# Performance work log

Hardware: AMD Instinct MI355X
Metric: run time of the kernel (lower is better)

## Reference

```python
import jax, jax.numpy as jnp
import numpy as np

NUM_HEADS = 16
ROPE_THETA = 10000.0


def _rope(x, pos):
    # x: [B, H, S, d_k], pos: [S]
    d_k = x.shape[-1]
    inv_freq = ROPE_THETA ** (-jnp.arange(0, d_k, 2, dtype=x.dtype) / d_k)  # [d_k/2]
    ang = pos[:, None].astype(x.dtype) * inv_freq[None, :]  # [S, d_k/2]
    cos, sin = jnp.cos(ang), jnp.sin(ang)
    x1 = x[..., 0::2]
    x2 = x[..., 1::2]
    r1 = x1 * cos - x2 * sin
    r2 = x1 * sin + x2 * cos
    return jnp.stack([r1, r2], axis=-1).reshape(x.shape)


def setup_inputs() -> dict:
    key = jax.random.key(0)
    kx, kq, kk, kv = jax.random.split(key, 4)
    B, S, D = 2, 2048, 2048
    scale = 1.0 / np.sqrt(D)
    x = jax.random.normal(kx, (B, S, D), dtype=jnp.float32)
    wq = jax.random.normal(kq, (D, D), dtype=jnp.float32) * scale
    wk = jax.random.normal(kk, (D, D), dtype=jnp.float32) * scale
    wv = jax.random.normal(kv, (D, D), dtype=jnp.float32) * scale
    return {"x": x, "wq": wq, "wk": wk, "wv": wv}


def reference(x, wq, wk, wv):
    B, S, D = x.shape
    H = NUM_HEADS
    d_k = D // H
    # QKV projections (Linear stores weight as [out, in]; y = x @ W^T)
    q = (x @ wq.T).reshape(B, S, H, d_k).transpose(0, 2, 1, 3)  # [B,H,S,dk]
    k = (x @ wk.T).reshape(B, S, H, d_k).transpose(0, 2, 1, 3)
    v = (x @ wv.T).reshape(B, S, H, d_k).transpose(0, 2, 1, 3)
    pos = jnp.arange(S)
    q = _rope(q, pos)
    k = _rope(k, pos)
    scores = jnp.einsum("bhqd,bhkd->bhqk", q, k) / jnp.sqrt(jnp.asarray(d_k, x.dtype))
    causal = jnp.tril(jnp.ones((S, S), dtype=bool))
    scores = jnp.where(causal, scores, jnp.asarray(-1e9, x.dtype))
    attn = jax.nn.softmax(scores, axis=-1)
    out = jnp.einsum("bhqk,bhkd->bhqd", attn, v)  # [B,H,S,dk]
    return out.transpose(0, 2, 1, 3).reshape(B, S, D)
```

## Files before the change

kernel.cpp:

```cpp
#include <hip/hip_runtime.h>
#include <stdint.h>

typedef unsigned short u16;
typedef __bf16 bf16x8 __attribute__((ext_vector_type(8)));
typedef float f32x4 __attribute__((ext_vector_type(4)));
typedef float f32x16 __attribute__((ext_vector_type(16)));

#define NHEADS 16
#define DKH    128
#define SEQ    2048
#define DMODEL 2048
#define NBATCH 2

typedef const __attribute__((address_space(1))) void* gas1_t;
typedef __attribute__((address_space(3))) void* las3_t;

__device__ __forceinline__ void gload_lds16(const void* g, void* l) {
  __builtin_amdgcn_global_load_lds((gas1_t)(uintptr_t)g,
                                   (las3_t)(uint32_t)(uintptr_t)l, 16, 0, 0);
}

__device__ __forceinline__ u16 bf(float f) {
  return __builtin_bit_cast(u16, (__bf16)f);
}

__device__ __forceinline__ uint32_t pk(float lo, float hi) {
  return (uint32_t)bf(lo) | ((uint32_t)bf(hi) << 16);
}

__device__ __forceinline__ float lanebcast(int srclane, float v) {
  return __builtin_bit_cast(float,
      __builtin_amdgcn_ds_bpermute(srclane << 2, __builtin_bit_cast(int, v)));
}

__global__ __launch_bounds__(256) void cvt_all(const float* __restrict__ x,
                                               const float* __restrict__ wq,
                                               const float* __restrict__ wk,
                                               const float* __restrict__ wv,
                                               u16* __restrict__ xb,
                                               u16* __restrict__ wb) {
  int i = (blockIdx.x * 256 + threadIdx.x) * 4;
  const int NX = NBATCH * SEQ * DMODEL;
  const int NW = DMODEL * DMODEL;
  const float* src;
  u16* dst;
  int j;
  if (i < NX) { src = x; dst = xb; j = i; }
  else {
    int k = i - NX;
    int w = k / NW;
    j = k - w * NW;
    src = (w == 0) ? wq : (w == 1) ? wk : wv;
    dst = wb + (size_t)w * NW;
  }
  const float4 v = *(const float4*)(src + j);
  uint2 o;
  o.x = (uint32_t)bf(v.x) | ((uint32_t)bf(v.y) << 16);
  o.y = (uint32_t)bf(v.z) | ((uint32_t)bf(v.w) << 16);
  *(uint2*)(dst + j) = o;
}

__global__ __launch_bounds__(256) void rope_table(float2* __restrict__ tbl) {
  int i = blockIdx.x * 256 + threadIdx.x;
  int s = i >> 6, d2 = i & 63;
  const float kLog2Theta = 13.28771237954945f;
  float inv_freq = exp2f(-(float)d2 * (2.0f / 128.0f) * kLog2Theta);
  float ang = (float)s * inv_freq;
  tbl[i] = make_float2(cosf(ang), sinf(ang));
}

__global__ __launch_bounds__(256, 4) void gemm_qkv(const u16* __restrict__ Abf,
                                                   const u16* __restrict__ Wbf,
                                                   const float2* __restrict__ rope,
                                                   u16* __restrict__ qb,
                                                   u16* __restrict__ kb,
                                                   u16* __restrict__ vtb) {
  __shared__ u16 S[16384];
  u16* As = S;
  u16* Bs = S + 8192;
  const int tid = threadIdx.x;
  const int lane = tid & 63, wid = tid >> 6;
  const int wr = wid >> 1, wc = wid & 1;
  const int blk = blockIdx.x;
  const int m0 = (blk / 48) * 128;
  const int n0 = (blk % 48) * 128;
  const int lrow = lane & 15, lgrp = lane >> 4, lko = lgrp * 8;
  const int rswz = (lrow & 7) << 3;

  const int srow = tid >> 3;
  const int scol = ((tid & 7) * 8) ^ (((tid >> 3) & 7) << 3);

  f32x4 acc[4][4] = {};

  for (int k0 = 0; k0 < DMODEL; k0 += 64) {
    __syncthreads();
#pragma unroll
    for (int c = 0; c < 4; ++c) {
      gload_lds16(Abf + (size_t)(m0 + c * 32 + srow) * DMODEL + k0 + scol,
                  As + (c * 256 + tid) * 8);
      gload_lds16(Wbf + (size_t)(n0 + c * 32 + srow) * DMODEL + k0 + scol,
                  Bs + (c * 256 + tid) * 8);
    }
    __syncthreads();
#pragma unroll
    for (int kk = 0; kk < 2; ++kk) {
      const int rc = (kk * 32 + lko) ^ rswz;
      bf16x8 a[4], b[4];
#pragma unroll
      for (int m = 0; m < 4; ++m)
        a[m] = *(const bf16x8*)(As + (wr * 64 + m * 16 + lrow) * 64 + rc);
#pragma unroll
      for (int n = 0; n < 4; ++n)
        b[n] = *(const bf16x8*)(Bs + (wc * 64 + n * 16 + lrow) * 64 + rc);
#pragma unroll
      for (int m = 0; m < 4; ++m)
#pragma unroll
        for (int n = 0; n < 4; ++n)
          acc[m][n] = __builtin_amdgcn_mfma_f32_16x16x32_bf16(a[m], b[n], acc[m][n], 0, 0, 0);
    }
  }

  const int sel = n0 >> 11;
  const float qsc = 0.08838834764831845f * 1.44269504088896341f;

  if (sel != 2) {
#pragma unroll
    for (int m = 0; m < 4; ++m) {
      int grow0 = m0 + wr * 64 + m * 16 + (lgrp << 2);
#pragma unroll
      for (int n = 0; n < 4; ++n) {
        int gcol = n0 + wc * 64 + n * 16 + lrow;
        int within = gcol & 2047;
        int h_ = within >> 7, d_ = within & 127;
#pragma unroll
        for (int j = 0; j < 4; ++j) {
          float v = acc[m][n][j];
          int r = grow0 + j;
          int b_ = r >> 11, s_ = r & 2047;
          int bh = b_ * NHEADS + h_;
          float part = __shfl_xor(v, 1);
          float2 cs2 = rope[s_ * 64 + (d_ >> 1)];
          v = (d_ & 1) ? (part * cs2.y + v * cs2.x) : (v * cs2.x - part * cs2.y);
          if (sel == 0) v *= qsc;
          u16* dq = sel ? kb : qb;
          dq[((size_t)bh * SEQ + s_) * DKH + d_] = bf(v);
        }
      }
    }
  } else {
    __syncthreads();
#pragma unroll
    for (int m = 0; m < 4; ++m) {
      int sl0 = wr * 64 + m * 16 + (lgrp << 2);
#pragma unroll
      for (int n = 0; n < 4; ++n) {
        int dcol = wc * 64 + n * 16 + lrow;
        const int dx = (dcol & 7) << 4;
#pragma unroll
        for (int j = 0; j < 4; ++j)
          S[dcol * 128 + ((sl0 + j) ^ dx)] = bf(acc[m][n][j]);
      }
    }
    __syncthreads();
    const int b_ = m0 >> 11, s0 = m0 & 2047;
    const int h_ = (n0 >> 7) & 15;
    const int bh = b_ * NHEADS + h_;
    const int d = tid >> 1, hf = tid & 1;
    const int dx = (d & 7) << 4;
    u16* grow = vtb + ((size_t)bh * DKH + d) * SEQ + s0 + hf * 64;
#pragma unroll
    for (int g = 0; g < 8; ++g) {
      bf16x8 v8 = *(const bf16x8*)(S + d * 128 + ((hf * 64 + g * 8) ^ dx));
      *(bf16x8*)(grow + g * 8) = v8;
    }
  }
}

__global__ __launch_bounds__(256, 2) void attn_fwd(const u16* __restrict__ qb,
                                                   const u16* __restrict__ kb,
                                                   const u16* __restrict__ vtb,
                                                   float* __restrict__ out) {
  __shared__ u16 Ks[2][64 * 128];
  __shared__ u16 Vs[2][128 * 64];
  const int tid = threadIdx.x, lane = tid & 63, wid = tid >> 6;
  const int blk = blockIdx.x;
  const int r_ = blk & 255, half = blk >> 8;
  const int bh = r_ & 31;
  const int pairidx = r_ >> 5;
  const int chunk = half ? (15 - pairidx) : pairidx;
  const int qln = lane & 31, hi = lane >> 5;
  const int hi4 = hi << 2, hi8 = hi << 3;
  const int kswz = (qln & 15) << 3;
  const int vswz = (qln & 7) << 3;

  const int krow_l = tid >> 4;
  const int kcol = (((tid & 15) ^ (tid >> 4)) << 3);
  const int vrow_l = tid >> 3;
  const int vcol = (((tid & 7) ^ ((tid >> 3) & 7)) << 3);

  const int b_ = bh >> 4, h_ = bh & 15;
  const size_t kbase = (size_t)bh * SEQ;
  const size_t vbase = (size_t)bh * DKH;

#define STAGE_KV(bufi, kv_)                                                  \
  _Pragma("unroll")                                                          \
  for (int c = 0; c < 4; ++c) {                                              \
    gload_lds16(kb + (kbase + (kv_) + c * 16 + krow_l) * DKH + kcol,         \
                &Ks[bufi][(c * 256 + tid) * 8]);                             \
    gload_lds16(vtb + (vbase + c * 32 + vrow_l) * SEQ + (kv_) + vcol,        \
                &Vs[bufi][(c * 256 + tid) * 8]);                             \
  }

  const int q0w = chunk * 128 + wid * 32;
  const int qglob = q0w + qln;

  bf16x8 qa[8];
#pragma unroll
  for (int kd = 0; kd < 8; ++kd)
    qa[kd] = *(const bf16x8*)(qb + (kbase + q0w + qln) * DKH + kd * 16 + hi8);

  f32x16 o[4] = {};
  float mrun = -1e30f, lrun = 0.f;

  const int nt = 2 * chunk + 2;

  STAGE_KV(0, 0);
  __syncthreads();

#pragma unroll 1
  for (int t = 0; t < nt; ++t) {
    const int cur = t & 1;
    if (t + 1 < nt) { STAGE_KV(cur ^ 1, (t + 1) * 64); }
    const int kv0 = t * 64;

    if (kv0 <= q0w + 31) {
      const u16* Kb = &Ks[cur][0];
      const u16* Vb = &Vs[cur][0];

      f32x16 sfv[2] = {};
      __builtin_amdgcn_s_setprio(1);
#pragma unroll
      for (int kd = 0; kd < 8; ++kd)
#pragma unroll
        for (int st = 0; st < 2; ++st) {
          bf16x8 kf = *(const bf16x8*)(Kb + (st * 32 + qln) * 128 +
                                       ((kd * 16 + hi8) ^ kswz));
          sfv[st] = __builtin_amdgcn_mfma_f32_32x32x16_bf16(kf, qa[kd], sfv[st], 0, 0, 0);
        }
      __builtin_amdgcn_s_setprio(0);

      if (kv0 + 63 > q0w) {
#pragma unroll
        for (int st = 0; st < 2; ++st)
#pragma unroll
          for (int r = 0; r < 16; ++r)
            if (kv0 + st * 32 + ((r & 3) + 8 * (r >> 2)) + hi4 > qglob)
              sfv[st][r] = -1e30f;
      }

      float tm[16];
#pragma unroll
      for (int r = 0; r < 16; ++r) tm[r] = fmaxf(sfv[0][r], sfv[1][r]);
#pragma unroll
      for (int r = 0; r < 8; ++r) tm[r] = fmaxf(tm[r], tm[r + 8]);
#pragma unroll
      for (int r = 0; r < 4; ++r) tm[r] = fmaxf(tm[r], tm[r + 4]);
      float m_ = fmaxf(fmaxf(tm[0], tm[1]), fmaxf(tm[2], tm[3]));
      m_ = fmaxf(m_, __shfl_xor(m_, 32));

      if (__any(m_ > mrun + 11.5f)) {
        float mnew = fmaxf(mrun, m_);
        float alpha = __builtin_amdgcn_exp2f(mrun - mnew);
        mrun = mnew;
        lrun *= alpha;
#pragma unroll
        for (int r = 0; r < 16; ++r) {
          float ar = lanebcast((r & 3) + 8 * (r >> 2) + hi4, alpha);
          o[0][r] *= ar; o[1][r] *= ar; o[2][r] *= ar; o[3][r] *= ar;
        }
      }

#pragma unroll
      for (int st = 0; st < 2; ++st)
#pragma unroll
        for (int r = 0; r < 16; ++r)
          sfv[st][r] = __builtin_amdgcn_exp2f(sfv[st][r] - mrun);
      float ts[16];
#pragma unroll
      for (int r = 0; r < 16; ++r) ts[r] = sfv[0][r] + sfv[1][r];
#pragma unroll
      for (int r = 0; r < 8; ++r) ts[r] += ts[r + 8];
#pragma unroll
      for (int r = 0; r < 4; ++r) ts[r] += ts[r + 4];
      float sum = (ts[0] + ts[1]) + (ts[2] + ts[3]);
      sum += __shfl_xor(sum, 32);
      lrun += sum;

      __builtin_amdgcn_s_setprio(1);
#pragma unroll
      for (int ks = 0; ks < 4; ++ks) {
        const int st = ks >> 1, rb = (ks & 1) * 8;
        uint32_t w0 = pk(sfv[st][rb + 0], sfv[st][rb + 1]);
        uint32_t w1 = pk(sfv[st][rb + 2], sfv[st][rb + 3]);
        uint32_t w2 = pk(sfv[st][rb + 4], sfv[st][rb + 5]);
        uint32_t w3 = pk(sfv[st][rb + 6], sfv[st][rb + 7]);
        uint32_t s0 = hi ? w0 : w2, s1 = hi ? w1 : w3;
        uint32_t r0 = (uint32_t)__shfl_xor((int)s0, 32);
        uint32_t r1 = (uint32_t)__shfl_xor((int)s1, 32);
        union { uint32_t u[4]; bf16x8 v; } pa;
        pa.u[0] = hi ? r0 : w0;
        pa.u[1] = hi ? r1 : w1;
        pa.u[2] = hi ? w2 : r0;
        pa.u[3] = hi ? w3 : r1;
#pragma unroll
        for (int d0 = 0; d0 < 4; ++d0) {
          bf16x8 vf = *(const bf16x8*)(Vb + (d0 * 32 + qln) * 64 +
                                       ((ks * 16 + hi8) ^ vswz));
          o[d0] = __builtin_amdgcn_mfma_f32_32x32x16_bf16(pa.v, vf, o[d0], 0, 0, 0);
        }
      }
      __builtin_amdgcn_s_setprio(0);
    }

    __syncthreads();
  }

  float inv = 1.f / lrun;
#pragma unroll
  for (int r = 0; r < 16; ++r) {
    const int qr = (r & 3) + 8 * (r >> 2) + hi4;
    float invr = lanebcast(qr, inv);
    float* op = out + ((size_t)b_ * SEQ + q0w + qr) * DMODEL + h_ * DKH + qln;
    op[0]  = o[0][r] * invr;
    op[32] = o[1][r] * invr;
    op[64] = o[2][r] * invr;
    op[96] = o[3][r] * invr;
  }
#undef STAGE_KV
}

extern "C" void kernel_launch(void* const* d_in, const int* in_sizes, int n_in,
                              void* d_out, int out_size, void* d_ws, size_t ws_size,
                              hipStream_t stream) {
  const float* x  = (const float*)d_in[0];
  const float* wq = (const float*)d_in[1];
  const float* wk = (const float*)d_in[2];
  const float* wv = (const float*)d_in[3];
  float* out = (float*)d_out;
  char* ws = (char*)d_ws;

  u16* xb  = (u16*)(ws);
  u16* wb  = (u16*)(ws + 16777216);
  u16* qb  = (u16*)(ws + 41943040);
  u16* kb  = (u16*)(ws + 58720256);
  u16* vtb = (u16*)(ws + 75497472);

  float2* rope = (float2*)d_out;

  rope_table<<<512, 256, 0, stream>>>(rope);
  cvt_all<<<20480, 256, 0, stream>>>(x, wq, wk, wv, xb, wb);
  gemm_qkv<<<1536, 256, 0, stream>>>(xb, wb, rope, qb, kb, vtb);
  attn_fwd<<<512, 256, 0, stream>>>(qb, kb, vtb, out);
}
```

Baseline: 191.7 us.

## Enlarge QKV GEMM tiles to 256x256 with double-buffered LDS prefetch

Rewrites the QKV projection GEMM to use 256x256 output tiles per 512-thread block, with a double-buffered LDS pipeline that prefetches the next K slice while MFMAs run. It also raises MFMA priority via setprio and remaps block indices across groups of eight for better L2 locality. The epilogues are adjusted for the larger tile, including a V transpose that now spans two heads. The aim is more operand reuse per load and latency hidden by overlap, at the cost of 128KB of LDS, heavier register pressure and many barriers per iteration.

Measured after the change: 213.2 us. 11.2% more time.

```diff
diff --git a/kernel.cpp b/kernel.cpp
--- a/kernel.cpp
+++ b/kernel.cpp
@@ -69,64 +69,107 @@
   tbl[i] = make_float2(cosf(ang), sinf(ang));
 }
 
-__global__ __launch_bounds__(256, 4) void gemm_qkv(const u16* __restrict__ Abf,
+__global__ __launch_bounds__(512, 2) void gemm_qkv(const u16* __restrict__ Abf,
                                                    const u16* __restrict__ Wbf,
                                                    const float2* __restrict__ rope,
                                                    u16* __restrict__ qb,
                                                    u16* __restrict__ kb,
                                                    u16* __restrict__ vtb) {
-  __shared__ u16 S[16384];
-  u16* As = S;
-  u16* Bs = S + 8192;
+  __shared__ u16 SH[65536];
+
   const int tid = threadIdx.x;
   const int lane = tid & 63, wid = tid >> 6;
-  const int wr = wid >> 1, wc = wid & 1;
-  const int blk = blockIdx.x;
-  const int m0 = (blk / 48) * 128;
-  const int n0 = (blk % 48) * 128;
-  const int lrow = lane & 15, lgrp = lane >> 4, lko = lgrp * 8;
+  const int wr = wid >> 2, wc = wid & 3;
+  const int g = (blockIdx.x & 7) * 48 + (blockIdx.x >> 3);
+  const int m0 = (g / 24) * 256;
+  const int n0 = (g % 24) * 256;
+  const int lrow = lane & 15, lgrp = lane >> 4;
   const int rswz = (lrow & 7) << 3;
 
-  const int srow = tid >> 3;
-  const int scol = ((tid & 7) * 8) ^ (((tid >> 3) & 7) << 3);
-
-  f32x4 acc[4][4] = {};
-
-  for (int k0 = 0; k0 < DMODEL; k0 += 64) {
-    __syncthreads();
-#pragma unroll
-    for (int c = 0; c < 4; ++c) {
-      gload_lds16(Abf + (size_t)(m0 + c * 32 + srow) * DMODEL + k0 + scol,
-                  As + (c * 256 + tid) * 8);
-      gload_lds16(Wbf + (size_t)(n0 + c * 32 + srow) * DMODEL + k0 + scol,
-                  Bs + (c * 256 + tid) * 8);
-    }
-    __syncthreads();
-#pragma unroll
-    for (int kk = 0; kk < 2; ++kk) {
-      const int rc = (kk * 32 + lko) ^ rswz;
-      bf16x8 a[4], b[4];
-#pragma unroll
-      for (int m = 0; m < 4; ++m)
-        a[m] = *(const bf16x8*)(As + (wr * 64 + m * 16 + lrow) * 64 + rc);
-#pragma unroll
-      for (int n = 0; n < 4; ++n)
-        b[n] = *(const bf16x8*)(Bs + (wc * 64 + n * 16 + lrow) * 64 + rc);
-#pragma unroll
-      for (int m = 0; m < 4; ++m)
-#pragma unroll
-        for (int n = 0; n < 4; ++n)
-          acc[m][n] = __builtin_amdgcn_mfma_f32_16x16x32_bf16(a[m], b[n], acc[m][n], 0, 0, 0);
-    }
-  }
-
-  const int sel = n0 >> 11;
+  const int srow8 = tid >> 3;
+  const int scol = ((tid & 7) ^ (srow8 & 7)) << 3;
+
+  const u16* const Ag = Abf + (size_t)m0 * DMODEL;
+  const u16* const Bg = Wbf + (size_t)n0 * DMODEL;
+
+  f32x4 acc[8][4] = {};
+
+#define STAGE_A(buf, k0_, c)                                                  \
+  gload_lds16(Ag + (size_t)((c) * 64 + srow8) * DMODEL + (k0_) + scol,        \
+              SH + (buf) * 16384 + (c) * 4096 + tid * 8)
+#define STAGE_B(buf, k0_, c)                                                  \
+  gload_lds16(Bg + (size_t)((c) * 64 + srow8) * DMODEL + (k0_) + scol,        \
+              SH + 32768 + (buf) * 16384 + (c) * 4096 + tid * 8)
+#define LDA(base, row, kk)                                                    \
+  (*(const bf16x8*)((base) + (row) * 64 + (((kk) * 32 + lgrp * 8) ^ rswz)))
+#define MFMA16(mh)                                                            \
+  __builtin_amdgcn_s_setprio(1);                                              \
+  _Pragma("unroll") for (int m_ = 0; m_ < 4; ++m_)                            \
+    _Pragma("unroll") for (int n_ = 0; n_ < 4; ++n_)                          \
+      acc[(mh) * 4 + m_][n_] = __builtin_amdgcn_mfma_f32_16x16x32_bf16(       \
+          a[m_], b[n_], acc[(mh) * 4 + m_][n_], 0, 0, 0);                     \
+  __builtin_amdgcn_s_setprio(0)
+
+#pragma unroll
+  for (int c = 0; c < 4; ++c) { STAGE_A(0, 0, c); STAGE_B(0, 0, c); }
+  asm volatile("s_waitcnt vmcnt(0)" ::: "memory");
+  __builtin_amdgcn_s_barrier();
+
+  const int NT = DMODEL / 64;
+#pragma unroll 1
+  for (int t = 0; t < NT; ++t) {
+    const int cur = t & 1, nxt = cur ^ 1;
+    const int k1 = (t + 1) * 64;
+    const u16* Ab = SH + cur * 16384;
+    const u16* Bb = SH + 32768 + cur * 16384;
+    const bool pf = (t + 1 < NT);
+    bf16x8 a[4], b[4];
+
+#pragma unroll
+    for (int m = 0; m < 4; ++m) a[m] = LDA(Ab, wr * 128 + m * 16 + lrow, 0);
+#pragma unroll
+    for (int n = 0; n < 4; ++n) b[n] = LDA(Bb, wc * 64 + n * 16 + lrow, 0);
+    if (pf) { STAGE_A(nxt, k1, 0); STAGE_A(nxt, k1, 1);
+              STAGE_B(nxt, k1, 0); STAGE_B(nxt, k1, 1); }
+    __builtin_amdgcn_s_barrier();
+    MFMA16(0);
+    __builtin_amdgcn_s_barrier();
+
+#pragma unroll
+    for (int m = 0; m < 4; ++m) a[m] = LDA(Ab, wr * 128 + 64 + m * 16 + lrow, 0);
+    if (pf) { STAGE_A(nxt, k1, 2); STAGE_A(nxt, k1, 3);
+              STAGE_B(nxt, k1, 2); STAGE_B(nxt, k1, 3); }
+    __builtin_amdgcn_s_barrier();
+    MFMA16(1);
+    __builtin_amdgcn_s_barrier();
+
+#pragma unroll
+    for (int m = 0; m < 4; ++m) a[m] = LDA(Ab, wr * 128 + m * 16 + lrow, 1);
+#pragma unroll
+    for (int n = 0; n < 4; ++n) b[n] = LDA(Bb, wc * 64 + n * 16 + lrow, 1);
+    __builtin_amdgcn_s_barrier();
+    MFMA16(0);
+    __builtin_amdgcn_s_barrier();
+
+#pragma unroll
+    for (int m = 0; m < 4; ++m) a[m] = LDA(Ab, wr * 128 + 64 + m * 16 + lrow, 1);
+    __builtin_amdgcn_s_barrier();
+    MFMA16(1);
+    asm volatile("s_waitcnt vmcnt(0)" ::: "memory");
+    __builtin_amdgcn_s_barrier();
+  }
+#undef STAGE_A
+#undef STAGE_B
+#undef LDA
+#undef MFMA16
+
+  const int sel = (n0 >= 4096) ? 2 : (n0 >= 2048 ? 1 : 0);
   const float qsc = 0.08838834764831845f * 1.44269504088896341f;
 
   if (sel != 2) {
 #pragma unroll
-    for (int m = 0; m < 4; ++m) {
-      int grow0 = m0 + wr * 64 + m * 16 + (lgrp << 2);
+    for (int m = 0; m < 8; ++m) {
+      int grow0 = m0 + wr * 128 + m * 16 + (lgrp << 2);
 #pragma unroll
       for (int n = 0; n < 4; ++n) {
         int gcol = n0 + wc * 64 + n * 16 + lrow;
@@ -150,28 +193,28 @@
   } else {
     __syncthreads();
 #pragma unroll
-    for (int m = 0; m < 4; ++m) {
-      int sl0 = wr * 64 + m * 16 + (lgrp << 2);
+    for (int m = 0; m < 8; ++m) {
+      int sl0 = wr * 128 + m * 16 + (lgrp << 2);
 #pragma unroll
       for (int n = 0; n < 4; ++n) {
         int dcol = wc * 64 + n * 16 + lrow;
-        const int dx = (dcol & 7) << 4;
+        const int dx = (dcol & 7) << 3;
 #pragma unroll
         for (int j = 0; j < 4; ++j)
-          S[dcol * 128 + ((sl0 + j) ^ dx)] = bf(acc[m][n][j]);
+          SH[dcol * 256 + ((sl0 + j) ^ dx)] = bf(acc[m][n][j]);
       }
     }
     __syncthreads();
     const int b_ = m0 >> 11, s0 = m0 & 2047;
-    const int h_ = (n0 >> 7) & 15;
-    const int bh = b_ * NHEADS + h_;
+    const int h0 = (n0 & 2047) >> 7;
     const int d = tid >> 1, hf = tid & 1;
-    const int dx = (d & 7) << 4;
-    u16* grow = vtb + ((size_t)bh * DKH + d) * SEQ + s0 + hf * 64;
-#pragma unroll
-    for (int g = 0; g < 8; ++g) {
-      bf16x8 v8 = *(const bf16x8*)(S + d * 128 + ((hf * 64 + g * 8) ^ dx));
-      *(bf16x8*)(grow + g * 8) = v8;
+    const int dx = (d & 7) << 3;
+    const int bh = b_ * NHEADS + h0 + (d >> 7);
+    u16* grow = vtb + ((size_t)bh * DKH + (d & 127)) * SEQ + s0 + hf * 128;
+#pragma unroll
+    for (int gi = 0; gi < 16; ++gi) {
+      bf16x8 v8 = *(const bf16x8*)(SH + d * 256 + ((hf * 128 + gi * 8) ^ dx));
+      *(bf16x8*)(grow + gi * 8) = v8;
     }
   }
 }
@@ -359,6 +402,6 @@
 
   rope_table<<<512, 256, 0, stream>>>(rope);
   cvt_all<<<20480, 256, 0, stream>>>(x, wq, wk, wv, xb, wb);
-  gemm_qkv<<<1536, 256, 0, stream>>>(xb, wb, rope, qb, kb, vtb);
+  gemm_qkv<<<384, 512, 0, stream>>>(xb, wb, rope, qb, kb, vtb);
   attn_fwd<<<512, 256, 0, stream>>>(qb, kb, vtb, out);
 }
```

## Triple-buffer QKV GEMM with 256x128 tiles, 512 threads and XCD-aware block mapping

Applied to the files above, without the earlier changes.

Rewrites the QKV projection GEMM to use 256x128 block tiles with 8 waves and a three-stage LDS ring buffer. Global-to-LDS prefetches for tile t+2 are interleaved with the MFMA phases, using vmcnt waits and raw barriers, with raised wave priority around the MFMAs. Blocks are remapped so each XCD handles a contiguous range of N tiles, which should improve L2 reuse of the weights. The V-transpose epilogue is adapted to the larger M tile. This costs more LDS (144KB per block) and lower occupancy, and the hand-managed waitcnt logic risks races if the counts are wrong.

Measured after the change: 199.3 us. 4.0% more time.

```diff
diff --git a/kernel.cpp b/kernel.cpp
--- a/kernel.cpp
+++ b/kernel.cpp
@@ -69,58 +69,102 @@
   tbl[i] = make_float2(cosf(ang), sinf(ang));
 }
 
-__global__ __launch_bounds__(256, 4) void gemm_qkv(const u16* __restrict__ Abf,
+__global__ __launch_bounds__(512, 2) void gemm_qkv(const u16* __restrict__ Abf,
                                                    const u16* __restrict__ Wbf,
                                                    const float2* __restrict__ rope,
                                                    u16* __restrict__ qb,
                                                    u16* __restrict__ kb,
                                                    u16* __restrict__ vtb) {
-  __shared__ u16 S[16384];
-  u16* As = S;
-  u16* Bs = S + 8192;
+  __shared__ u16 SH[73728];
+
   const int tid = threadIdx.x;
   const int lane = tid & 63, wid = tid >> 6;
   const int wr = wid >> 1, wc = wid & 1;
-  const int blk = blockIdx.x;
-  const int m0 = (blk / 48) * 128;
-  const int n0 = (blk % 48) * 128;
-  const int lrow = lane & 15, lgrp = lane >> 4, lko = lgrp * 8;
+  const int xcd = blockIdx.x & 7, i_ = blockIdx.x >> 3;
+  const int m0 = (i_ / 6) * 256;
+  const int n0 = (xcd * 6 + (i_ % 6)) * 128;
+  const int lrow = lane & 15, lgrp = lane >> 4;
   const int rswz = (lrow & 7) << 3;
 
-  const int srow = tid >> 3;
-  const int scol = ((tid & 7) * 8) ^ (((tid >> 3) & 7) << 3);
+  const int srow8 = tid >> 3;
+  const int scol = ((tid & 7) ^ (srow8 & 7)) << 3;
+
+  const u16* const Ag = Abf + (size_t)m0 * DMODEL;
+  const u16* const Bg = Wbf + (size_t)n0 * DMODEL;
 
   f32x4 acc[4][4] = {};
 
-  for (int k0 = 0; k0 < DMODEL; k0 += 64) {
-    __syncthreads();
-#pragma unroll
-    for (int c = 0; c < 4; ++c) {
-      gload_lds16(Abf + (size_t)(m0 + c * 32 + srow) * DMODEL + k0 + scol,
-                  As + (c * 256 + tid) * 8);
-      gload_lds16(Wbf + (size_t)(n0 + c * 32 + srow) * DMODEL + k0 + scol,
-                  Bs + (c * 256 + tid) * 8);
-    }
-    __syncthreads();
-#pragma unroll
-    for (int kk = 0; kk < 2; ++kk) {
-      const int rc = (kk * 32 + lko) ^ rswz;
-      bf16x8 a[4], b[4];
-#pragma unroll
-      for (int m = 0; m < 4; ++m)
-        a[m] = *(const bf16x8*)(As + (wr * 64 + m * 16 + lrow) * 64 + rc);
+#define STAGE_A(buf, k0_, c)                                                  \
+  gload_lds16(Ag + (size_t)((c) * 64 + srow8) * DMODEL + (k0_) + scol,        \
+              SH + (buf) + (c) * 4096 + tid * 8)
+#define STAGE_B(buf, k0_, c)                                                  \
+  gload_lds16(Bg + (size_t)((c) * 64 + srow8) * DMODEL + (k0_) + scol,        \
+              SH + (buf) + 16384 + (c) * 4096 + tid * 8)
+#define LD8(base, row, kk)                                                    \
+  (*(const bf16x8*)((base) + (row) * 64 + (((kk) * 32 + lgrp * 8) ^ rswz)))
+
+#pragma unroll
+  for (int c = 0; c < 4; ++c) STAGE_A(0, 0, c);
+#pragma unroll
+  for (int c = 0; c < 2; ++c) STAGE_B(0, 0, c);
+#pragma unroll
+  for (int c = 0; c < 4; ++c) STAGE_A(24576, 64, c);
+#pragma unroll
+  for (int c = 0; c < 2; ++c) STAGE_B(24576, 64, c);
+  asm volatile("s_waitcnt vmcnt(6)" ::: "memory");
+  __builtin_amdgcn_s_barrier();
+
+  int bR = 0, bM = 24576, bW = 49152;
+  const int NT = DMODEL / 64;
+
+#pragma unroll 1
+  for (int t = 0; t < NT; ++t) {
+    const u16* Ar = SH + bR;
+    const u16* Br = SH + bR + 16384;
+    const int k2 = (t + 2) * 64;
+    const bool pf = (t + 2 < NT);
+    bf16x8 a[4], b[4];
+
+#pragma unroll
+    for (int m = 0; m < 4; ++m) a[m] = LD8(Ar, wr * 64 + m * 16 + lrow, 0);
+#pragma unroll
+    for (int n = 0; n < 4; ++n) b[n] = LD8(Br, wc * 64 + n * 16 + lrow, 0);
+    if (pf) { STAGE_A(bW, k2, 0); STAGE_A(bW, k2, 1); STAGE_A(bW, k2, 2); }
+    __builtin_amdgcn_s_barrier();
+    __builtin_amdgcn_s_setprio(1);
+#pragma unroll
+    for (int m = 0; m < 4; ++m)
 #pragma unroll
       for (int n = 0; n < 4; ++n)
-        b[n] = *(const bf16x8*)(Bs + (wc * 64 + n * 16 + lrow) * 64 + rc);
-#pragma unroll
-      for (int m = 0; m < 4; ++m)
-#pragma unroll
-        for (int n = 0; n < 4; ++n)
-          acc[m][n] = __builtin_amdgcn_mfma_f32_16x16x32_bf16(a[m], b[n], acc[m][n], 0, 0, 0);
-    }
-  }
-
-  const int sel = n0 >> 11;
+        acc[m][n] = __builtin_amdgcn_mfma_f32_16x16x32_bf16(a[m], b[n], acc[m][n], 0, 0, 0);
+    __builtin_amdgcn_s_setprio(0);
+    __builtin_amdgcn_s_barrier();
+
+#pragma unroll
+    for (int m = 0; m < 4; ++m) a[m] = LD8(Ar, wr * 64 + m * 16 + lrow, 1);
+#pragma unroll
+    for (int n = 0; n < 4; ++n) b[n] = LD8(Br, wc * 64 + n * 16 + lrow, 1);
+    if (pf) { STAGE_A(bW, k2, 3); STAGE_B(bW, k2, 0); STAGE_B(bW, k2, 1); }
+    __builtin_amdgcn_s_barrier();
+    __builtin_amdgcn_s_setprio(1);
+#pragma unroll
+    for (int m = 0; m < 4; ++m)
+#pragma unroll
+      for (int n = 0; n < 4; ++n)
+        acc[m][n] = __builtin_amdgcn_mfma_f32_16x16x32_bf16(a[m], b[n], acc[m][n], 0, 0, 0);
+    __builtin_amdgcn_s_setprio(0);
+    if (t < NT - 2) asm volatile("s_waitcnt vmcnt(6)" ::: "memory");
+    else            asm volatile("s_waitcnt vmcnt(0)" ::: "memory");
+    __builtin_amdgcn_s_barrier();
+
+    int tmp = bR; bR = bM; bM = bW; bW = tmp;
+  }
+#undef STAGE_A
+#undef STAGE_B
+#undef LD8
+
+  const int np = n0 >> 7;
+  const int sel = (np >= 32) ? 2 : (np >= 16 ? 1 : 0);
   const float qsc = 0.08838834764831845f * 1.44269504088896341f;
 
   if (sel != 2) {
@@ -155,22 +199,22 @@
 #pragma unroll
       for (int n = 0; n < 4; ++n) {
         int dcol = wc * 64 + n * 16 + lrow;
-        const int dx = (dcol & 7) << 4;
+        const int dx = (dcol & 7) << 3;
 #pragma unroll
         for (int j = 0; j < 4; ++j)
-          S[dcol * 128 + ((sl0 + j) ^ dx)] = bf(acc[m][n][j]);
+          SH[dcol * 256 + ((sl0 + j) ^ dx)] = bf(acc[m][n][j]);
       }
     }
     __syncthreads();
     const int b_ = m0 >> 11, s0 = m0 & 2047;
-    const int h_ = (n0 >> 7) & 15;
+    const int h_ = np & 15;
     const int bh = b_ * NHEADS + h_;
-    const int d = tid >> 1, hf = tid & 1;
-    const int dx = (d & 7) << 4;
-    u16* grow = vtb + ((size_t)bh * DKH + d) * SEQ + s0 + hf * 64;
+    const int d = tid >> 2, seg = tid & 3;
+    const int dxr = (d & 7) << 3;
+    u16* grow = vtb + ((size_t)bh * DKH + d) * SEQ + s0 + seg * 64;
 #pragma unroll
     for (int g = 0; g < 8; ++g) {
-      bf16x8 v8 = *(const bf16x8*)(S + d * 128 + ((hf * 64 + g * 8) ^ dx));
+      bf16x8 v8 = *(const bf16x8*)(SH + d * 256 + ((seg * 64 + g * 8) ^ dxr));
       *(bf16x8*)(grow + g * 8) = v8;
     }
   }
@@ -359,6 +403,6 @@
 
   rope_table<<<512, 256, 0, stream>>>(rope);
   cvt_all<<<20480, 256, 0, stream>>>(x, wq, wk, wv, xb, wb);
-  gemm_qkv<<<1536, 256, 0, stream>>>(xb, wb, rope, qb, kb, vtb);
+  gemm_qkv<<<768, 512, 0, stream>>>(xb, wb, rope, qb, kb, vtb);
   attn_fwd<<<512, 256, 0, stream>>>(qb, kb, vtb, out);
 }
```

## Read K/V directly from global in attention and fuse rope table into convert

Applied to the files above, without the earlier changes.

The attention kernel drops its double-buffered LDS staging of K and V tiles. Each wave now loads its MFMA fragments straight from global memory, and each wave exits its loop early instead of sitting through block-wide barriers. This removes the LDS traffic and __syncthreads, but every wave re-reads K/V from L2/HBM with no sharing across the four waves, and the loads are no longer prefetched ahead of use. Separately, rope table generation is folded into the convert kernel as extra blocks, which saves one launch.

After: 282.1 us. +47.1%, slower.

```diff
diff --git a/kernel.cpp b/kernel.cpp
--- a/kernel.cpp
+++ b/kernel.cpp
@@ -38,8 +38,19 @@
                                                const float* __restrict__ wk,
                                                const float* __restrict__ wv,
                                                u16* __restrict__ xb,
-                                               u16* __restrict__ wb) {
-  int i = (blockIdx.x * 256 + threadIdx.x) * 4;
+                                               u16* __restrict__ wb,
+                                               float2* __restrict__ rope) {
+  const int gb = blockIdx.x;
+  if (gb >= 20480) {
+    int i = (gb - 20480) * 256 + threadIdx.x;
+    int s = i >> 6, d2 = i & 63;
+    const float kLog2Theta = 13.28771237954945f;
+    float inv_freq = exp2f(-(float)d2 * (2.0f / 128.0f) * kLog2Theta);
+    float ang = (float)s * inv_freq;
+    rope[i] = make_float2(cosf(ang), sinf(ang));
+    return;
+  }
+  int i = (gb * 256 + threadIdx.x) * 4;
   const int NX = NBATCH * SEQ * DMODEL;
   const int NW = DMODEL * DMODEL;
   const float* src;
@@ -58,15 +69,6 @@
   o.x = (uint32_t)bf(v.x) | ((uint32_t)bf(v.y) << 16);
   o.y = (uint32_t)bf(v.z) | ((uint32_t)bf(v.w) << 16);
   *(uint2*)(dst + j) = o;
-}
-
-__global__ __launch_bounds__(256) void rope_table(float2* __restrict__ tbl) {
-  int i = blockIdx.x * 256 + threadIdx.x;
-  int s = i >> 6, d2 = i & 63;
-  const float kLog2Theta = 13.28771237954945f;
-  float inv_freq = exp2f(-(float)d2 * (2.0f / 128.0f) * kLog2Theta);
-  float ang = (float)s * inv_freq;
-  tbl[i] = make_float2(cosf(ang), sinf(ang));
 }
 
 __global__ __launch_bounds__(256, 4) void gemm_qkv(const u16* __restrict__ Abf,
@@ -180,8 +182,6 @@
                                                    const u16* __restrict__ kb,
                                                    const u16* __restrict__ vtb,
                                                    float* __restrict__ out) {
-  __shared__ u16 Ks[2][64 * 128];
-  __shared__ u16 Vs[2][128 * 64];
   const int tid = threadIdx.x, lane = tid & 63, wid = tid >> 6;
   const int blk = blockIdx.x;
   const int r_ = blk & 255, half = blk >> 8;
@@ -190,26 +190,10 @@
   const int chunk = half ? (15 - pairidx) : pairidx;
   const int qln = lane & 31, hi = lane >> 5;
   const int hi4 = hi << 2, hi8 = hi << 3;
-  const int kswz = (qln & 15) << 3;
-  const int vswz = (qln & 7) << 3;
-
-  const int krow_l = tid >> 4;
-  const int kcol = (((tid & 15) ^ (tid >> 4)) << 3);
-  const int vrow_l = tid >> 3;
-  const int vcol = (((tid & 7) ^ ((tid >> 3) & 7)) << 3);
 
   const int b_ = bh >> 4, h_ = bh & 15;
   const size_t kbase = (size_t)bh * SEQ;
-  const size_t vbase = (size_t)bh * DKH;
-
-#define STAGE_KV(bufi, kv_)                                                  \
-  _Pragma("unroll")                                                          \
-  for (int c = 0; c < 4; ++c) {                                              \
-    gload_lds16(kb + (kbase + (kv_) + c * 16 + krow_l) * DKH + kcol,         \
-                &Ks[bufi][(c * 256 + tid) * 8]);                             \
-    gload_lds16(vtb + (vbase + c * 32 + vrow_l) * SEQ + (kv_) + vcol,        \
-                &Vs[bufi][(c * 256 + tid) * 8]);                             \
-  }
+  const u16* const Vgb = vtb + (size_t)bh * DKH * SEQ;
 
   const int q0w = chunk * 128 + wid * 32;
   const int qglob = q0w + qln;
@@ -224,105 +208,97 @@
 
   const int nt = 2 * chunk + 2;
 
-  STAGE_KV(0, 0);
-  __syncthreads();
-
 #pragma unroll 1
   for (int t = 0; t < nt; ++t) {
-    const int cur = t & 1;
-    if (t + 1 < nt) { STAGE_KV(cur ^ 1, (t + 1) * 64); }
     const int kv0 = t * 64;
-
-    if (kv0 <= q0w + 31) {
-      const u16* Kb = &Ks[cur][0];
-      const u16* Vb = &Vs[cur][0];
-
-      f32x16 sfv[2] = {};
-      __builtin_amdgcn_s_setprio(1);
-#pragma unroll
-      for (int kd = 0; kd < 8; ++kd)
-#pragma unroll
-        for (int st = 0; st < 2; ++st) {
-          bf16x8 kf = *(const bf16x8*)(Kb + (st * 32 + qln) * 128 +
-                                       ((kd * 16 + hi8) ^ kswz));
-          sfv[st] = __builtin_amdgcn_mfma_f32_32x32x16_bf16(kf, qa[kd], sfv[st], 0, 0, 0);
-        }
-      __builtin_amdgcn_s_setprio(0);
-
-      if (kv0 + 63 > q0w) {
-#pragma unroll
-        for (int st = 0; st < 2; ++st)
-#pragma unroll
-          for (int r = 0; r < 16; ++r)
-            if (kv0 + st * 32 + ((r & 3) + 8 * (r >> 2)) + hi4 > qglob)
-              sfv[st][r] = -1e30f;
-      }
-
-      float tm[16];
-#pragma unroll
-      for (int r = 0; r < 16; ++r) tm[r] = fmaxf(sfv[0][r], sfv[1][r]);
-#pragma unroll
-      for (int r = 0; r < 8; ++r) tm[r] = fmaxf(tm[r], tm[r + 8]);
-#pragma unroll
-      for (int r = 0; r < 4; ++r) tm[r] = fmaxf(tm[r], tm[r + 4]);
-      float m_ = fmaxf(fmaxf(tm[0], tm[1]), fmaxf(tm[2], tm[3]));
-      m_ = fmaxf(m_, __shfl_xor(m_, 32));
-
-      if (__any(m_ > mrun + 11.5f)) {
-        float mnew = fmaxf(mrun, m_);
-        float alpha = __builtin_amdgcn_exp2f(mrun - mnew);
-        mrun = mnew;
-        lrun *= alpha;
-#pragma unroll
-        for (int r = 0; r < 16; ++r) {
-          float ar = lanebcast((r & 3) + 8 * (r >> 2) + hi4, alpha);
-          o[0][r] *= ar; o[1][r] *= ar; o[2][r] *= ar; o[3][r] *= ar;
-        }
-      }
-
+    if (kv0 > q0w + 31) break;
+
+    const u16* Kg = kb + (kbase + kv0) * DKH;
+    const u16* Vg = Vgb + kv0;
+
+    f32x16 sfv[2] = {};
+    __builtin_amdgcn_s_setprio(1);
+#pragma unroll
+    for (int kd = 0; kd < 8; ++kd)
+#pragma unroll
+      for (int st = 0; st < 2; ++st) {
+        bf16x8 kf = *(const bf16x8*)(Kg + (size_t)(st * 32 + qln) * DKH +
+                                     kd * 16 + hi8);
+        sfv[st] = __builtin_amdgcn_mfma_f32_32x32x16_bf16(kf, qa[kd], sfv[st], 0, 0, 0);
+      }
+    __builtin_amdgcn_s_setprio(0);
+
+    if (kv0 + 63 > q0w) {
 #pragma unroll
       for (int st = 0; st < 2; ++st)
 #pragma unroll
         for (int r = 0; r < 16; ++r)
-          sfv[st][r] = __builtin_amdgcn_exp2f(sfv[st][r] - mrun);
-      float ts[16];
-#pragma unroll
-      for (int r = 0; r < 16; ++r) ts[r] = sfv[0][r] + sfv[1][r];
-#pragma unroll
-      for (int r = 0; r < 8; ++r) ts[r] += ts[r + 8];
-#pragma unroll
-      for (int r = 0; r < 4; ++r) ts[r] += ts[r + 4];
-      float sum = (ts[0] + ts[1]) + (ts[2] + ts[3]);
-      sum += __shfl_xor(sum, 32);
-      lrun += sum;
-
-      __builtin_amdgcn_s_setprio(1);
-#pragma unroll
-      for (int ks = 0; ks < 4; ++ks) {
-        const int st = ks >> 1, rb = (ks & 1) * 8;
-        uint32_t w0 = pk(sfv[st][rb + 0], sfv[st][rb + 1]);
-        uint32_t w1 = pk(sfv[st][rb + 2], sfv[st][rb + 3]);
-        uint32_t w2 = pk(sfv[st][rb + 4], sfv[st][rb + 5]);
-        uint32_t w3 = pk(sfv[st][rb + 6], sfv[st][rb + 7]);
-        uint32_t s0 = hi ? w0 : w2, s1 = hi ? w1 : w3;
-        uint32_t r0 = (uint32_t)__shfl_xor((int)s0, 32);
-        uint32_t r1 = (uint32_t)__shfl_xor((int)s1, 32);
-        union { uint32_t u[4]; bf16x8 v; } pa;
-        pa.u[0] = hi ? r0 : w0;
-        pa.u[1] = hi ? r1 : w1;
-        pa.u[2] = hi ? w2 : r0;
-        pa.u[3] = hi ? w3 : r1;
-#pragma unroll
-        for (int d0 = 0; d0 < 4; ++d0) {
-          bf16x8 vf = *(const bf16x8*)(Vb + (d0 * 32 + qln) * 64 +
-                                       ((ks * 16 + hi8) ^ vswz));
-          o[d0] = __builtin_amdgcn_mfma_f32_32x32x16_bf16(pa.v, vf, o[d0], 0, 0, 0);
-        }
-      }
-      __builtin_amdgcn_s_setprio(0);
-    }
-
-    __syncthreads();
+          if (kv0 + st * 32 + ((r & 3) + 8 * (r >> 2)) + hi4 > qglob)
+            sfv[st][r] = -1e30f;
+    }
+
+    float tm[16];
+#pragma unroll
+    for (int r = 0; r < 16; ++r) tm[r] = fmaxf(sfv[0][r], sfv[1][r]);
+#pragma unroll
+    for (int r = 0; r < 8; ++r) tm[r] = fmaxf(tm[r], tm[r + 8]);
+#pragma unroll
+    for (int r = 0; r < 4; ++r) tm[r] = fmaxf(tm[r], tm[r + 4]);
+    float m_ = fmaxf(fmaxf(tm[0], tm[1]), fmaxf(tm[2], tm[3]));
+    m_ = fmaxf(m_, __shfl_xor(m_, 32));
+
+    if (__any(m_ > mrun + 11.5f)) {
+      float mnew = fmaxf(mrun, m_);
+      float alpha = __builtin_amdgcn_exp2f(mrun - mnew);
+      mrun = mnew;
+      lrun *= alpha;
+#pragma unroll
+      for (int r = 0; r < 16; ++r) {
+        float ar = lanebcast((r & 3) + 8 * (r >> 2) + hi4, alpha);
+        o[0][r] *= ar; o[1][r] *= ar; o[2][r] *= ar; o[3][r] *= ar;
+      }
+    }
+
+#pragma unroll
+    for (int st = 0; st < 2; ++st)
+#pragma unroll
+      for (int r = 0; r < 16; ++r)
+        sfv[st][r] = __builtin_amdgcn_exp2f(sfv[st][r] - mrun);
+    float ts[16];
+#pragma unroll
+    for (int r = 0; r < 16; ++r) ts[r] = sfv[0][r] + sfv[1][r];
+#pragma unroll
+    for (int r = 0; r < 8; ++r) ts[r] += ts[r + 8];
+#pragma unroll
+    for (int r = 0; r < 4; ++r) ts[r] += ts[r + 4];
+    float sum = (ts[0] + ts[1]) + (ts[2] + ts[3]);
+    sum += __shfl_xor(sum, 32);
+    lrun += sum;
+
+    __builtin_amdgcn_s_setprio(1);
+#pragma unroll
+    for (int ks = 0; ks < 4; ++ks) {
+      const int st = ks >> 1, rb = (ks & 1) * 8;
+      uint32_t w0 = pk(sfv[st][rb + 0], sfv[st][rb + 1]);
+      uint32_t w1 = pk(sfv[st][rb + 2], sfv[st][rb + 3]);
+      uint32_t w2 = pk(sfv[st][rb + 4], sfv[st][rb + 5]);
+      uint32_t w3 = pk(sfv[st][rb + 6], sfv[st][rb + 7]);
+      uint32_t s0 = hi ? w0 : w2, s1 = hi ? w1 : w3;
+      uint32_t r0 = (uint32_t)__shfl_xor((int)s0, 32);
+      uint32_t r1 = (uint32_t)__shfl_xor((int)s1, 32);
+      union { uint32_t u[4]; bf16x8 v; } pa;
+      pa.u[0] = hi ? r0 : w0;
+      pa.u[1] = hi ? r1 : w1;
+      pa.u[2] = hi ? w2 : r0;
+      pa.u[3] = hi ? w3 : r1;
+#pragma unroll
+      for (int d0 = 0; d0 < 4; ++d0) {
+        bf16x8 vf = *(const bf16x8*)(Vg + (size_t)(d0 * 32 + qln) * SEQ +
+                                     ks * 16 + hi8);
+        o[d0] = __builtin_amdgcn_mfma_f32_32x32x16_bf16(pa.v, vf, o[d0], 0, 0, 0);
+      }
+    }
+    __builtin_amdgcn_s_setprio(0);
   }
 
   float inv = 1.f / lrun;
@@ -336,7 +312,6 @@
     op[64] = o[2][r] * invr;
     op[96] = o[3][r] * invr;
   }
-#undef STAGE_KV
 }
 
 extern "C" void kernel_launch(void* const* d_in, const int* in_sizes, int n_in,
@@ -357,8 +332,7 @@
 
   float2* rope = (float2*)d_out;
 
-  rope_table<<<512, 256, 0, stream>>>(rope);
-  cvt_all<<<20480, 256, 0, stream>>>(x, wq, wk, wv, xb, wb);
+  cvt_all<<<20992, 256, 0, stream>>>(x, wq, wk, wv, xb, wb, rope);
   gemm_qkv<<<1536, 256, 0, stream>>>(xb, wb, rope, qb, kb, vtb);
   attn_fwd<<<512, 256, 0, stream>>>(qb, kb, vtb, out);
 }
```
